# Kernel tuning notes

Measured on AMD Instinct MI355X. Metric: run time of the kernel, lower is better.

The kernel has to match this reference:

```python
import jax, jax.numpy as jnp
import numpy as np

EPS = 1e-08
B, ATT, RELA = 16, 64, 128
RNN, HID = 1024, 512


def setup_inputs() -> dict:
    key = jax.random.key(0)
    k = jax.random.split(key, 8)
    obj_vecs_e = jax.random.normal(k[0], (B, ATT, RNN), dtype=jnp.float32)
    rela_feats = jax.random.normal(k[1], (B, RELA, RNN), dtype=jnp.float32)
    p_rela_feats = jax.random.normal(k[2], (B, RELA, HID), dtype=jnp.float32)
    obj_rela_masks = jax.random.randint(k[3], (B, ATT, RELA), 0, 2, dtype=jnp.int32)
    # learned params: obj2att Linear(RNN -> HID), alpha_net Linear(HID -> 1)
    W_obj = jax.random.normal(k[4], (RNN, HID), dtype=jnp.float32) / np.sqrt(RNN)
    b_obj = jax.random.normal(k[5], (HID,), dtype=jnp.float32) * 0.01
    w_alpha = jax.random.normal(k[6], (HID,), dtype=jnp.float32) / np.sqrt(HID)
    b_alpha = jax.random.normal(k[7], (), dtype=jnp.float32) * 0.01
    return {
        "obj_vecs_e": obj_vecs_e,
        "rela_feats": rela_feats,
        "p_rela_feats": p_rela_feats,
        "W_obj": W_obj,
        "b_obj": b_obj,
        "w_alpha": w_alpha,
        "b_alpha": b_alpha,
        "obj_rela_masks": obj_rela_masks,
    }


def reference(obj_vecs_e, rela_feats, p_rela_feats, W_obj, b_obj, w_alpha, b_alpha, obj_rela_masks):
    # att_obj: [B, ATT, HID]
    att_obj = jnp.einsum("bad,dh->bah", obj_vecs_e, W_obj) + b_obj
    # broadcast add: [B, ATT, RELA, HID]
    dot = jnp.tanh(p_rela_feats[:, None, :, :] + att_obj[:, :, None, :])
    # alpha_net: scores [B, ATT, RELA]
    scores = jnp.einsum("barh,h->bar", dot, w_alpha) + b_alpha
    weight = jax.nn.softmax(scores, axis=-1)
    mask = obj_rela_masks.astype(weight.dtype)
    weight = weight * mask
    weight = weight / (jnp.sum(weight, axis=-1, keepdims=True) + EPS)
    # weighted sum of relation features: [B, ATT, RNN]
    att_res = jnp.einsum("bar,brd->bad", weight, rela_feats)
    return att_res
```

## Files before the change

kernel.cpp:

```cpp
#include <hip/hip_runtime.h>


constexpr int B_   = 16;
constexpr int ATT  = 64;
constexpr int RELA = 128;
constexpr int RNN  = 1024;
constexpr int HID  = 512;
constexpr int M_   = B_ * ATT;
constexpr float EPS_ = 1e-8f;
constexpr float K2LN = 2.885390081777927f;
constexpr int RT  = 8;
constexpr int NRT = RELA / RT;
constexpr int HG  = 64;
constexpr int NHG = HID / HG;
constexpr int HW  = 16;

typedef short bf16x8 __attribute__((ext_vector_type(8)));
typedef float f32x4  __attribute__((ext_vector_type(4)));

__device__ __forceinline__ unsigned short f2bf(float f) {
    unsigned u = __float_as_uint(f);
    u += 0x7FFFu + ((u >> 16) & 1u);
    return (unsigned short)(u >> 16);
}

__global__ __launch_bounds__(256) void k0_pre(const float* __restrict__ A,
                                              const float* __restrict__ W,
                                              unsigned short* __restrict__ Abf,
                                              unsigned short* __restrict__ WT) {
    const int bid = blockIdx.x;
    const int tid = threadIdx.x;
    if (bid < 512) {
        const size_t idx = ((size_t)bid * 256 + tid) << 3;
        const float4 f0 = *reinterpret_cast<const float4*>(&A[idx]);
        const float4 f1 = *reinterpret_cast<const float4*>(&A[idx + 4]);
        unsigned short us[8] = {f2bf(f0.x), f2bf(f0.y), f2bf(f0.z), f2bf(f0.w),
                                f2bf(f1.x), f2bf(f1.y), f2bf(f1.z), f2bf(f1.w)};
        *reinterpret_cast<uint4*>(&Abf[idx]) = *reinterpret_cast<uint4*>(us);
    } else {
        __shared__ float Ts[64][68];
        const int wb = bid - 512;
        const int k0 = (wb >> 3) << 6, n0 = (wb & 7) << 6;
        #pragma unroll
        for (int i = 0; i < 4; ++i) {
            const int r = (tid >> 4) + (i << 4);
            const int c4 = (tid & 15) << 2;
            *reinterpret_cast<float4*>(&Ts[r][c4]) =
                *reinterpret_cast<const float4*>(&W[(size_t)(k0 + r) * HID + n0 + c4]);
        }
        __syncthreads();
        const int n = tid >> 2, kq = (tid & 3) << 4;
        unsigned short us[16];
        #pragma unroll
        for (int e = 0; e < 16; ++e)
            us[e] = f2bf(Ts[kq + e][n]);
        unsigned short* dst = &WT[(size_t)(n0 + n) * RNN + k0 + kq];
        *reinterpret_cast<uint4*>(dst)     = *reinterpret_cast<uint4*>(us);
        *reinterpret_cast<uint4*>(dst + 8) = *reinterpret_cast<uint4*>(us + 8);
    }
}

__global__ __launch_bounds__(256) void k1_mfma(const unsigned short* __restrict__ Abf,
                                               const unsigned short* __restrict__ WT,
                                               const float* __restrict__ b_obj,
                                               float* __restrict__ Eq) {
    const int tid = threadIdx.x;
    const int lane = tid & 63;
    const int wave = tid >> 6;
    const int m0 = (blockIdx.x << 5) + ((wave >> 1) << 4);
    const int n0 = (blockIdx.y << 5) + ((wave & 1) << 4);
    const int row  = lane & 15;
    const int koff = (lane >> 4) << 3;
    const unsigned short* ap = &Abf[(size_t)(m0 + row) * RNN + koff];
    const unsigned short* bp = &WT[(size_t)(n0 + row) * RNN + koff];
    f32x4 acc0 = {}, acc1 = {};
    #pragma unroll 4
    for (int k = 0; k < RNN; k += 64) {
        const bf16x8 a0 = *reinterpret_cast<const bf16x8*>(ap + k);
        const bf16x8 b0 = *reinterpret_cast<const bf16x8*>(bp + k);
        const bf16x8 a1 = *reinterpret_cast<const bf16x8*>(ap + k + 32);
        const bf16x8 b1 = *reinterpret_cast<const bf16x8*>(bp + k + 32);
        acc0 = __builtin_amdgcn_mfma_f32_16x16x32_bf16(a0, b0, acc0, 0, 0, 0);
        acc1 = __builtin_amdgcn_mfma_f32_16x16x32_bf16(a1, b1, acc1, 0, 0, 0);
    }
    const int dcol = lane & 15;
    const int drow0 = (lane >> 4) << 2;
    const float bias = b_obj[n0 + dcol];
    #pragma unroll
    for (int v = 0; v < 4; ++v)
        Eq[(size_t)(m0 + drow0 + v) * HID + n0 + dcol] =
            __builtin_amdgcn_exp2f((acc0[v] + acc1[v] + bias) * K2LN);
}

__global__ __launch_bounds__(256, 8) void k2a_scores(const float* __restrict__ Eq,
                                                     const float* __restrict__ p_rela,
                                                     const float* __restrict__ w_alpha,
                                                     float* __restrict__ partials) {
    const int b  = blockIdx.x;
    const int rt = blockIdx.y;
    const int hg = blockIdx.z;
    const int tid = threadIdx.x;
    const int lane = tid & 63;
    const int wave = tid >> 6;

    __shared__ float ps[RT][HG];
    __shared__ float wws[HG];
    __shared__ float red[4][RT][ATT];

    if (tid < 128) {
        const int row = tid >> 4, c4 = (tid & 15) << 2;
        float4 v = *reinterpret_cast<const float4*>(
            &p_rela[((size_t)b * RELA + rt * RT + row) * HID + hg * HG + c4]);
        v.x = __builtin_amdgcn_exp2f(v.x * K2LN);
        v.y = __builtin_amdgcn_exp2f(v.y * K2LN);
        v.z = __builtin_amdgcn_exp2f(v.z * K2LN);
        v.w = __builtin_amdgcn_exp2f(v.w * K2LN);
        *reinterpret_cast<float4*>(&ps[row][c4]) = v;
    } else if (tid < 144) {
        const int c4 = (tid - 128) << 2;
        float4 w = *reinterpret_cast<const float4*>(&w_alpha[hg * HG + c4]);
        w.x *= -2.f; w.y *= -2.f; w.z *= -2.f; w.w *= -2.f;
        *reinterpret_cast<float4*>(&wws[c4]) = w;
    }
    const int hbase = hg * HG + wave * HW;
    float4 eq[4];
    #pragma unroll
    for (int i = 0; i < 4; ++i)
        eq[i] = *reinterpret_cast<const float4*>(&Eq[(size_t)((b << 6) + lane) * HID + hbase + (i << 2)]);
    __syncthreads();

    float acc[RT] = {};
    #pragma unroll
    for (int i = 0; i < 4; ++i) {
        const float qq[4] = {eq[i].x, eq[i].y, eq[i].z, eq[i].w};
        const float4 w4 = *reinterpret_cast<const float4*>(&wws[wave * HW + (i << 2)]);
        const float ww[4] = {w4.x, w4.y, w4.z, w4.w};
        #pragma unroll
        for (int r = 0; r < RT; ++r) {
            const float4 p4 = *reinterpret_cast<const float4*>(&ps[r][wave * HW + (i << 2)]);
            const float pp[4] = {p4.x, p4.y, p4.z, p4.w};
            #pragma unroll
            for (int j = 0; j < 4; ++j) {
                const float e = pp[j] * qq[j];
                acc[r] = fmaf(ww[j], __builtin_amdgcn_rcpf(e + 1.f), acc[r]);
            }
        }
    }

    #pragma unroll
    for (int r = 0; r < RT; ++r)
        red[wave][r][lane] = acc[r];
    __syncthreads();

    const int a = tid & 63, rg = tid >> 6;
    float2 o;
    o.x = red[0][rg * 2][a] + red[1][rg * 2][a] + red[2][rg * 2][a] + red[3][rg * 2][a];
    o.y = red[0][rg * 2 + 1][a] + red[1][rg * 2 + 1][a] + red[2][rg * 2 + 1][a] + red[3][rg * 2 + 1][a];
    const size_t ba = (size_t)(b << 6) + a;
    *reinterpret_cast<float2*>(&partials[(ba * NHG + hg) * RELA + rt * RT + rg * 2]) = o;
}

__global__ __launch_bounds__(256) void k2b_softmax(const float* __restrict__ partials,
                                                   const int* __restrict__ masks,
                                                   float* __restrict__ weight) {
    const int tid = threadIdx.x;
    const int lane = tid & 63;
    const int wave = tid >> 6;
    const int ba = (blockIdx.x << 2) + wave;

    const float* pp = &partials[(size_t)ba * NHG * RELA];
    float s0 = 0.f, s1 = 0.f;
    #pragma unroll
    for (int hs = 0; hs < NHG; ++hs) {
        s0 += pp[hs * RELA + lane];
        s1 += pp[hs * RELA + lane + 64];
    }

    float m = fmaxf(s0, s1);
    #pragma unroll
    for (int off = 32; off > 0; off >>= 1)
        m = fmaxf(m, __shfl_xor(m, off));
    const float e0 = __expf(s0 - m), e1 = __expf(s1 - m);
    float sum = e0 + e1;
    #pragma unroll
    for (int off = 32; off > 0; off >>= 1)
        sum += __shfl_xor(sum, off);
    const float inv = 1.f / sum;
    const float m0 = (float)masks[(size_t)ba * RELA + lane];
    const float m1 = (float)masks[(size_t)ba * RELA + lane + 64];
    const float w0 = e0 * inv * m0;
    const float w1 = e1 * inv * m1;
    float ms = w0 + w1;
    #pragma unroll
    for (int off = 32; off > 0; off >>= 1)
        ms += __shfl_xor(ms, off);
    const float inv2 = 1.f / (ms + EPS_);
    weight[(size_t)ba * RELA + lane]      = w0 * inv2;
    weight[(size_t)ba * RELA + lane + 64] = w1 * inv2;
}

__global__ __launch_bounds__(256) void k3_wsum(const float* __restrict__ weight,
                                               const float* __restrict__ rela,
                                               float* __restrict__ out) {
    const int b = blockIdx.x;
    const int d_base = blockIdx.y << 6;
    const int ah = blockIdx.z;
    const int tid = threadIdx.x;
    const int col = tid & 15;
    const int la0 = (tid >> 4) << 1;

    __shared__ float ws_s[32][132];
    __shared__ float rs[32 * 64];
    #pragma unroll
    for (int i = 0; i < 4; ++i) {
        const int fi = tid + (i << 8);
        const int a = fi >> 5, r0 = (fi & 31) << 2;
        *reinterpret_cast<float4*>(&ws_s[a][r0]) =
            *reinterpret_cast<const float4*>(&weight[((size_t)b * ATT + (ah << 5) + a) * RELA + r0]);
    }
    float4 acc[2] = {};
    for (int rc = 0; rc < 4; ++rc) {
        __syncthreads();
        #pragma unroll
        for (int i = 0; i < 2; ++i) {
            const int fi = tid + (i << 8);
            const int rr = fi >> 4, c = fi & 15;
            *reinterpret_cast<float4*>(&rs[(rr << 6) + (c << 2)]) =
                *reinterpret_cast<const float4*>(&rela[((size_t)b * RELA + (rc << 5) + rr) * RNN + d_base + (c << 2)]);
        }
        __syncthreads();
        #pragma unroll 8
        for (int rr = 0; rr < 32; ++rr) {
            const float4 x = *reinterpret_cast<const float4*>(&rs[(rr << 6) + (col << 2)]);
            const int r = (rc << 5) + rr;
            #pragma unroll
            for (int ai = 0; ai < 2; ++ai) {
                const float wv = ws_s[la0 + ai][r];
                acc[ai].x = fmaf(wv, x.x, acc[ai].x);
                acc[ai].y = fmaf(wv, x.y, acc[ai].y);
                acc[ai].z = fmaf(wv, x.z, acc[ai].z);
                acc[ai].w = fmaf(wv, x.w, acc[ai].w);
            }
        }
    }
    #pragma unroll
    for (int ai = 0; ai < 2; ++ai)
        *reinterpret_cast<float4*>(
            &out[((size_t)(b << 6) + (ah << 5) + la0 + ai) * RNN + d_base + (col << 2)]) = acc[ai];
}

extern "C" void kernel_launch(void* const* d_in, const int* in_sizes, int n_in,
                              void* d_out, int out_size, void* d_ws, size_t ws_size,
                              hipStream_t stream) {
    const float* obj_vecs = (const float*)d_in[0];
    const float* rela     = (const float*)d_in[1];
    const float* p_rela   = (const float*)d_in[2];
    const float* W_obj    = (const float*)d_in[3];
    const float* b_obj    = (const float*)d_in[4];
    const float* w_alpha  = (const float*)d_in[5];
    const int*   masks    = (const int*)d_in[7];
    float* out = (float*)d_out;

    char* ws = (char*)d_ws;
    unsigned short* Abf = (unsigned short*)(ws);
    unsigned short* WT  = (unsigned short*)(ws + (2u << 20));
    float* Eq           = (float*)(ws + (3u << 20));
    float* partials     = (float*)(ws + (5u << 20));
    float* weight       = (float*)(ws + (9u << 20));

    k0_pre<<<dim3(640), 256, 0, stream>>>(obj_vecs, W_obj, Abf, WT);
    k1_mfma<<<dim3(M_ / 32, HID / 32), 256, 0, stream>>>(Abf, WT, b_obj, Eq);
    k2a_scores<<<dim3(B_, NRT, NHG), 256, 0, stream>>>(Eq, p_rela, w_alpha, partials);
    k2b_softmax<<<dim3(M_ / 4), 256, 0, stream>>>(partials, masks, weight);
    k3_wsum<<<dim3(B_, RNN / 64, 2), 256, 0, stream>>>(weight, rela, out);
}
```

Baseline: 47.51 us.

## Fuse softmax and mask normalization into weighted-sum kernel

Removes the separate softmax kernel and the intermediate weight buffer. Each wsum block now sums the per-hidden-group partial scores, computes the masked softmax in shared memory, then does the weighted sum. This saves a kernel launch and a global round trip of the weights. In exchange, the partial reduction and softmax are recomputed redundantly by every d-slice block, which adds many extra partials reads.

```diff
diff --git a/kernel.cpp b/kernel.cpp
--- a/kernel.cpp
+++ b/kernel.cpp
@@ -160,64 +160,65 @@
     *reinterpret_cast<float2*>(&partials[(ba * NHG + hg) * RELA + rt * RT + rg * 2]) = o;
 }
 
-__global__ __launch_bounds__(256) void k2b_softmax(const float* __restrict__ partials,
-                                                   const int* __restrict__ masks,
-                                                   float* __restrict__ weight) {
-    const int tid = threadIdx.x;
-    const int lane = tid & 63;
-    const int wave = tid >> 6;
-    const int ba = (blockIdx.x << 2) + wave;
-
-    const float* pp = &partials[(size_t)ba * NHG * RELA];
-    float s0 = 0.f, s1 = 0.f;
-    #pragma unroll
-    for (int hs = 0; hs < NHG; ++hs) {
-        s0 += pp[hs * RELA + lane];
-        s1 += pp[hs * RELA + lane + 64];
-    }
-
-    float m = fmaxf(s0, s1);
-    #pragma unroll
-    for (int off = 32; off > 0; off >>= 1)
-        m = fmaxf(m, __shfl_xor(m, off));
-    const float e0 = __expf(s0 - m), e1 = __expf(s1 - m);
-    float sum = e0 + e1;
-    #pragma unroll
-    for (int off = 32; off > 0; off >>= 1)
-        sum += __shfl_xor(sum, off);
-    const float inv = 1.f / sum;
-    const float m0 = (float)masks[(size_t)ba * RELA + lane];
-    const float m1 = (float)masks[(size_t)ba * RELA + lane + 64];
-    const float w0 = e0 * inv * m0;
-    const float w1 = e1 * inv * m1;
-    float ms = w0 + w1;
-    #pragma unroll
-    for (int off = 32; off > 0; off >>= 1)
-        ms += __shfl_xor(ms, off);
-    const float inv2 = 1.f / (ms + EPS_);
-    weight[(size_t)ba * RELA + lane]      = w0 * inv2;
-    weight[(size_t)ba * RELA + lane + 64] = w1 * inv2;
-}
-
-__global__ __launch_bounds__(256) void k3_wsum(const float* __restrict__ weight,
-                                               const float* __restrict__ rela,
-                                               float* __restrict__ out) {
+__global__ __launch_bounds__(256) void k3_softmax_wsum(const float* __restrict__ partials,
+                                                       const int* __restrict__ masks,
+                                                       const float* __restrict__ rela,
+                                                       float* __restrict__ out) {
     const int b = blockIdx.x;
     const int d_base = blockIdx.y << 6;
     const int ah = blockIdx.z;
     const int tid = threadIdx.x;
+    const int lane = tid & 63;
+    const int wave = tid >> 6;
+
+    __shared__ float ws_s[32][132];
+    __shared__ float rs[32 * 64];
+
+    #pragma unroll
+    for (int i = 0; i < 4; ++i) {
+        const int fi = tid + (i << 8);
+        const int la = fi >> 5, r4 = (fi & 31) << 2;
+        const float* pp = &partials[(size_t)((b << 6) + (ah << 5) + la) * NHG * RELA + r4];
+        float4 s = {0.f, 0.f, 0.f, 0.f};
+        #pragma unroll
+        for (int hg = 0; hg < NHG; ++hg) {
+            const float4 v = *reinterpret_cast<const float4*>(&pp[hg * RELA]);
+            s.x += v.x; s.y += v.y; s.z += v.z; s.w += v.w;
+        }
+        *reinterpret_cast<float4*>(&ws_s[la][r4]) = s;
+    }
+    __syncthreads();
+
+    #pragma unroll 1
+    for (int aa = 0; aa < 8; ++aa) {
+        const int la = (wave << 3) + aa;
+        const int ga = (b << 6) + (ah << 5) + la;
+        const float s0 = ws_s[la][lane], s1 = ws_s[la][lane + 64];
+        float m = fmaxf(s0, s1);
+        #pragma unroll
+        for (int off = 32; off > 0; off >>= 1)
+            m = fmaxf(m, __shfl_xor(m, off));
+        const float e0 = __expf(s0 - m), e1 = __expf(s1 - m);
+        float sum = e0 + e1;
+        #pragma unroll
+        for (int off = 32; off > 0; off >>= 1)
+            sum += __shfl_xor(sum, off);
+        const float inv = __builtin_amdgcn_rcpf(sum);
+        const float m0 = (float)masks[(size_t)ga * RELA + lane];
+        const float m1 = (float)masks[(size_t)ga * RELA + lane + 64];
+        const float w0 = e0 * inv * m0;
+        const float w1 = e1 * inv * m1;
+        float ms = w0 + w1;
+        #pragma unroll
+        for (int off = 32; off > 0; off >>= 1)
+            ms += __shfl_xor(ms, off);
+        const float inv2 = 1.f / (ms + EPS_);
+        ws_s[la][lane]      = w0 * inv2;
+        ws_s[la][lane + 64] = w1 * inv2;
+    }
+
     const int col = tid & 15;
     const int la0 = (tid >> 4) << 1;
-
-    __shared__ float ws_s[32][132];
-    __shared__ float rs[32 * 64];
-    #pragma unroll
-    for (int i = 0; i < 4; ++i) {
-        const int fi = tid + (i << 8);
-        const int a = fi >> 5, r0 = (fi & 31) << 2;
-        *reinterpret_cast<float4*>(&ws_s[a][r0]) =
-            *reinterpret_cast<const float4*>(&weight[((size_t)b * ATT + (ah << 5) + a) * RELA + r0]);
-    }
     float4 acc[2] = {};
     for (int rc = 0; rc < 4; ++rc) {
         __syncthreads();
@@ -266,11 +267,9 @@
     unsigned short* WT  = (unsigned short*)(ws + (2u << 20));
     float* Eq           = (float*)(ws + (3u << 20));
     float* partials     = (float*)(ws + (5u << 20));
-    float* weight       = (float*)(ws + (9u << 20));
 
     k0_pre<<<dim3(640), 256, 0, stream>>>(obj_vecs, W_obj, Abf, WT);
     k1_mfma<<<dim3(M_ / 32, HID / 32), 256, 0, stream>>>(Abf, WT, b_obj, Eq);
     k2a_scores<<<dim3(B_, NRT, NHG), 256, 0, stream>>>(Eq, p_rela, w_alpha, partials);
-    k2b_softmax<<<dim3(M_ / 4), 256, 0, stream>>>(partials, masks, weight);
-    k3_wsum<<<dim3(B_, RNN / 64, 2), 256, 0, stream>>>(weight, rela, out);
-}
+    k3_softmax_wsum<<<dim3(B_, RNN / 64, 2), 256, 0, stream>>>(partials, masks, rela, out);
+}
```

New measurement: 56.26 us. +18.4%, slower.
